# Kernel tuning notes

Hardware: AMD Instinct MI355X
Metric: run time of the kernel (lower is better)

The kernel has to match this reference:

```python
import jax, jax.numpy as jnp
import numpy as np
from jax import lax

POST_NMS_TOP_N = 1000   # cfg[cfg_key].RPN_POST_NMS_TOP_N
NMS_THRESH = 0.7        # cfg[cfg_key].RPN_NMS_THRESH
NEG = -1e9
B, N = 4, 65536


def setup_inputs() -> dict:
    key = jax.random.key(0)
    k0, k1, k2, k3, k4, k5, k6 = jax.random.split(key, 7)
    scores = jax.random.uniform(k0, (B, N), dtype=jnp.float32)
    # small deltas so exp(dw) stays in a realistic range
    bbox_deltas = 0.1 * jax.random.normal(k1, (B, N, 4), dtype=jnp.float32)
    # plausible anchor boxes inside a 1024x1024 image
    cx = jax.random.uniform(k2, (N,), minval=0.0, maxval=1024.0)
    cy = jax.random.uniform(k3, (N,), minval=0.0, maxval=1024.0)
    w = jax.random.uniform(k4, (N,), minval=16.0, maxval=256.0)
    h = jax.random.uniform(k5, (N,), minval=16.0, maxval=256.0)
    anchors = jnp.stack([cx - 0.5 * w, cy - 0.5 * h, cx + 0.5 * w, cy + 0.5 * h], axis=-1).astype(jnp.float32)
    im_info = jnp.tile(jnp.array([[1024.0, 1024.0, 1.0]], dtype=jnp.float32), (B, 1))
    ids = jax.random.randint(k6, (N,), 0, 5, dtype=jnp.int32)  # FPN level ids
    return {"scores": scores, "bbox_deltas": bbox_deltas, "anchors": anchors,
            "im_info": im_info, "ids": ids}


def _iou_one(box, boxes):
    # box [4], boxes [N,4]; mmcv convention (no +1)
    x1 = jnp.maximum(box[0], boxes[:, 0])
    y1 = jnp.maximum(box[1], boxes[:, 1])
    x2 = jnp.minimum(box[2], boxes[:, 2])
    y2 = jnp.minimum(box[3], boxes[:, 3])
    inter = jnp.clip(x2 - x1, 0.0) * jnp.clip(y2 - y1, 0.0)
    a1 = (box[2] - box[0]) * (box[3] - box[1])
    a2 = (boxes[:, 2] - boxes[:, 0]) * (boxes[:, 3] - boxes[:, 1])
    return inter / jnp.maximum(a1 + a2 - inter, 1e-6)


def _nms_single(boxes, scores, ids):
    # batched_nms: offset boxes by level id so levels never suppress each other
    max_c = jnp.max(boxes) + 1.0
    boxes_off = boxes + (ids.astype(boxes.dtype) * max_c)[:, None]

    def step(s, _):
        i = jnp.argmax(s)
        valid = s[i] > NEG * 0.5
        iou = _iou_one(boxes_off[i], boxes_off)
        s_new = jnp.where(iou > NMS_THRESH, NEG, s).at[i].set(NEG)
        sel = jnp.where(valid, boxes[i], jnp.zeros((4,), boxes.dtype))
        return s_new, sel

    _, sel = lax.scan(step, scores, None, length=POST_NMS_TOP_N)
    return sel  # [POST_NMS_TOP_N, 4], in descending score order (as batched_nms returns)


def _forward(scores, bbox_deltas, anchors, im_info, ids):
    ws = anchors[:, 2] - anchors[:, 0] + 1.0          # [N]
    hs = anchors[:, 3] - anchors[:, 1] + 1.0
    ctr_x = anchors[:, 0] + 0.5 * ws
    ctr_y = anchors[:, 1] + 0.5 * hs
    dx, dy, dw, dh = (bbox_deltas[..., 0], bbox_deltas[..., 1],
                      bbox_deltas[..., 2], bbox_deltas[..., 3])  # [B,N]
    pcx = dx * ws + ctr_x
    pcy = dy * hs + ctr_y
    pw = jnp.exp(dw) * ws
    ph = jnp.exp(dh) * hs
    proposals = jnp.stack([pcx - 0.5 * pw, pcy - 0.5 * ph,
                           pcx + 0.5 * pw, pcy + 0.5 * ph], axis=-1)  # [B,N,4]
    # clip_boxes: x in [0, w-1], y in [0, h-1]
    wmax = im_info[:, 1][:, None] - 1.0
    hmax = im_info[:, 0][:, None] - 1.0
    x1 = jnp.clip(proposals[..., 0], 0.0, wmax)
    y1 = jnp.clip(proposals[..., 1], 0.0, hmax)
    x2 = jnp.clip(proposals[..., 2], 0.0, wmax)
    y2 = jnp.clip(proposals[..., 3], 0.0, hmax)
    proposals = jnp.stack([x1, y1, x2, y2], axis=-1)
    # per-image batched NMS (greedy descending-score selection == sort + NMS)
    sel = jax.vmap(_nms_single, in_axes=(0, 0, None))(proposals, scores, ids)  # [B,topN,4]
    batch_col = jnp.broadcast_to(
        jnp.arange(scores.shape[0], dtype=sel.dtype)[:, None, None],
        (scores.shape[0], POST_NMS_TOP_N, 1))
    return jnp.concatenate([batch_col, sel], axis=-1)  # [B,topN,5]


def reference(scores, bbox_deltas, anchors, im_info, ids):
    return _forward(scores, bbox_deltas, anchors, im_info, ids)
```

## Files before the change

### kernel.cpp

```cpp
#include <hip/hip_runtime.h>
#include <stdint.h>

#define NB     65536
#define BATCH  4
#define TOPN   1000
#define MMAX   2048
#define NTILE  (MMAX / 64)
#define NPAIRS (NTILE * (NTILE + 1) / 2)
#define CAP    128
#define KSUP   8
#define UNC    128
#define THRESH 0.974f
#define NEGV   (-1e9f)
#define NMS_T  0.7f

#define OFF_CBLK   64
#define OFF_KRAW   1088
#define OFF_SBOX   263232
#define OFF_SLEV   394304
#define OFF_CNT2   427072
#define OFF_SUP    459840

__device__ __forceinline__ void decode_box(const float4* __restrict__ anchors4,
                                           const float4* __restrict__ deltas4,
                                           int b, int i, float wmax, float hmax,
                                           float& x1, float& y1, float& x2, float& y2) {
  float4 a = anchors4[i];
  float4 d = deltas4[(size_t)b * NB + i];
  float ws = a.z - a.x + 1.0f;
  float hs = a.w - a.y + 1.0f;
  float cx = a.x + 0.5f * ws;
  float cy = a.y + 0.5f * hs;
  float pcx = d.x * ws + cx;
  float pcy = d.y * hs + cy;
  float pw = expf(d.z) * ws;
  float ph = expf(d.w) * hs;
  x1 = pcx - 0.5f * pw; y1 = pcy - 0.5f * ph;
  x2 = pcx + 0.5f * pw; y2 = pcy + 0.5f * ph;
  x1 = fminf(fmaxf(x1, 0.0f), wmax);
  y1 = fminf(fmaxf(y1, 0.0f), hmax);
  x2 = fminf(fmaxf(x2, 0.0f), wmax);
  y2 = fminf(fmaxf(y2, 0.0f), hmax);
}

__device__ __forceinline__ uint32_t blockscan(uint32_t v, volatile uint32_t* wsum,
                                              int tid, uint32_t* total) {
  __syncthreads();
  int lane = tid & 63, wid = tid >> 6;
  uint32_t x = v;
  for (int off = 1; off < 64; off <<= 1) {
    uint32_t u = __shfl_up(x, off, 64);
    if (lane >= off) x += u;
  }
  if (lane == 63) wsum[wid] = x;
  __syncthreads();
  if (tid == 0) {
    uint32_t run = 0;
    for (int w = 0; w < 4; ++w) { uint32_t t = wsum[w]; wsum[w] = run; run += t; }
    wsum[4] = run;
  }
  __syncthreads();
  *total = wsum[4];
  return x - v + wsum[wid];
}

__global__ __launch_bounds__(256) void k_prep(const float* __restrict__ scores,
                                              unsigned long long* __restrict__ keys_raw,
                                              uint32_t* __restrict__ cnt_blk) {
  const int b = blockIdx.x >> 6;
  const int blk = blockIdx.x & 63;
  const int tid = threadIdx.x;
  __shared__ uint32_t wsum[5];
  const float4* s4 = (const float4*)scores + (size_t)b * (NB / 4) + (size_t)blk * 256 + tid;
  float4 s = *s4;
  float sc4[4] = {s.x, s.y, s.z, s.w};
  uint32_t cmask = 0, ccount = 0;
#pragma unroll
  for (int k = 0; k < 4; ++k)
    if (sc4[k] >= THRESH) { cmask |= (1u << k); ccount++; }
  uint32_t total;
  uint32_t p = blockscan(ccount, wsum, tid, &total);
  if (tid == 0) cnt_blk[blockIdx.x] = total;
  unsigned long long* dst = keys_raw + (size_t)blockIdx.x * CAP;
#pragma unroll
  for (int k = 0; k < 4; ++k) {
    if (cmask & (1u << k)) {
      if (p < (uint32_t)CAP) {
        int i = (blk << 10) + (tid << 2) + k;
        dst[p] = ((unsigned long long)(~__float_as_uint(sc4[k])) << 32) | (uint32_t)i;
      }
      p++;
    }
  }
}

__global__ __launch_bounds__(256) void k_rank(const uint32_t* __restrict__ cnt_blk,
                                              const unsigned long long* __restrict__ keys_raw,
                                              const float4* __restrict__ deltas4,
                                              const float4* __restrict__ anchors4,
                                              const float* __restrict__ im_info,
                                              const int* __restrict__ ids,
                                              uint32_t* ctrs,
                                              float4* sboxes, int* slev,
                                              uint32_t* cnt2) {
  const int b = blockIdx.y;
  const int r = blockIdx.x;
  const int tid = threadIdx.x;
  const int lane = tid & 63, wid = tid >> 6;
  __shared__ unsigned long long sk[MMAX];
  __shared__ uint32_t scnt[64], sbs[64];
  __shared__ uint32_t psum[256];
  __shared__ uint32_t meta[2];

  if (tid < 64) {
    uint32_t c = cnt_blk[b * 64 + tid];
    uint32_t cc = min(c, (uint32_t)CAP);
    scnt[tid] = cc;
    uint32_t x = cc;
    for (int off = 1; off < 64; off <<= 1) {
      uint32_t u = __shfl_up(x, off, 64);
      if (lane >= off) x += u;
    }
    sbs[tid] = x - cc;
    unsigned long long ov = __ballot(c > (uint32_t)CAP);
    if (tid == 63) { meta[0] = x; meta[1] = (ov != 0ULL) ? 1u : 0u; }
  }
  __syncthreads();
  uint32_t nsum = meta[0];
  int n = min((int)nsum, MMAX);
  uint32_t flag = meta[1] | ((nsum > (uint32_t)MMAX) ? 1u : 0u);
  if (r == 0 && tid == 0) {
    ctrs[b] = (uint32_t)n;
    ctrs[8 + b] = flag;
  }
  if (tid < 64) cnt2[(size_t)b * MMAX + r * 64 + tid] = 0u;
  {
    int k = tid >> 2, q = tid & 3;
    uint32_t cb = sbs[k], cc = scnt[k];
    const unsigned long long* src = keys_raw + ((size_t)b * 64 + k) * CAP;
    for (uint32_t o = q; o < cc; o += 4) {
      uint32_t d = cb + o;
      if (d < (uint32_t)MMAX) sk[d] = src[o];
    }
  }
  for (int i = tid; i < MMAX; i += 256) if (i >= n) sk[i] = ~0ULL;
  __syncthreads();
  int c = r * 64 + lane;
  uint32_t partial = 0;
  if (c < n) {
    unsigned long long myk = sk[c];
    const ulonglong2* p2 = (const ulonglong2*)(sk + (size_t)wid * 512);
    for (int it = 0; it < 256; it += 4) {
      ulonglong2 a = p2[it], bq = p2[it + 1], cq = p2[it + 2], dq = p2[it + 3];
      partial += (uint32_t)(a.x < myk) + (uint32_t)(a.y < myk) +
                 (uint32_t)(bq.x < myk) + (uint32_t)(bq.y < myk) +
                 (uint32_t)(cq.x < myk) + (uint32_t)(cq.y < myk) +
                 (uint32_t)(dq.x < myk) + (uint32_t)(dq.y < myk);
    }
  }
  psum[wid * 64 + lane] = partial;
  __syncthreads();
  if (tid < 64) {
    int cc = r * 64 + tid;
    if (cc < n) {
      uint32_t rank = psum[tid] + psum[64 + tid] + psum[128 + tid] + psum[192 + tid];
      if (rank < (uint32_t)MMAX) {
        unsigned long long key = sk[cc];
        int i = (int)(uint32_t)key;
        float wmax = im_info[b * 3 + 1] - 1.0f;
        float hmax = im_info[b * 3 + 0] - 1.0f;
        float x1, y1, x2, y2;
        decode_box(anchors4, deltas4, b, i, wmax, hmax, x1, y1, x2, y2);
        sboxes[(size_t)b * MMAX + rank] = make_float4(x1, y1, x2, y2);
        slev[(size_t)b * MMAX + rank] = ids[i];
      }
    }
  }
}

__global__ __launch_bounds__(64) void k_pairs(uint32_t* ctrs,
                                              const float4* __restrict__ sboxes,
                                              const int* __restrict__ slev,
                                              uint32_t* cnt2, int* suplist) {
  int b = blockIdx.y;
  int p = blockIdx.x;
  int tj = (int)((sqrtf(8.0f * (float)p + 1.0f) - 1.0f) * 0.5f);
  while ((tj + 1) * (tj + 2) / 2 <= p) ++tj;
  while (tj * (tj + 1) / 2 > p) --tj;
  int ti = p - tj * (tj + 1) / 2;
  int n = min((int)ctrs[b], MMAX);
  if (tj * 64 >= n) return;
  int lane = threadIdx.x;

  __shared__ float4 ib[64];
  __shared__ int il[64];
  int ii = ti * 64 + lane;
  if (ii < n) {
    ib[lane] = sboxes[(size_t)b * MMAX + ii];
    il[lane] = slev[(size_t)b * MMAX + ii];
  } else {
    il[lane] = -1;
  }
  int j = tj * 64 + lane;
  float4 J = make_float4(0.f, 0.f, 0.f, 0.f);
  int jl = -2;
  float aj = 0.0f;
  if (j < n) {
    J = sboxes[(size_t)b * MMAX + j];
    jl = slev[(size_t)b * MMAX + j];
    aj = (J.z - J.x) * (J.w - J.y);
  }
  __syncthreads();
  if (j < n) {
    int imax = (ti == tj) ? lane : 64;
    for (int k = 0; k < imax; ++k) {
      if (il[k] != jl) continue;
      float4 I = ib[k];
      float xx1 = fmaxf(I.x, J.x), yy1 = fmaxf(I.y, J.y);
      float xx2 = fminf(I.z, J.z), yy2 = fminf(I.w, J.w);
      float inter = fmaxf(xx2 - xx1, 0.0f) * fmaxf(yy2 - yy1, 0.0f);
      float ai = (I.z - I.x) * (I.w - I.y);
      float iou = inter / fmaxf((ai + aj) - inter, 1e-6f);
      if (iou > NMS_T) {
        uint32_t s = atomicAdd(&cnt2[(size_t)b * MMAX + j], 1u);
        if (s < (uint32_t)KSUP) suplist[((size_t)b * MMAX + j) * KSUP + s] = ti * 64 + k;
        else ctrs[8 + b] = 1u;
      }
    }
  }
}

__device__ __forceinline__ uint32_t scan_pair(uint32_t pairsum, volatile uint32_t* wsum,
                                              int tid, uint32_t* total_out) {
  int lane = tid & 63, wid = tid >> 6;
  uint32_t v = pairsum;
  for (int off = 1; off < 64; off <<= 1) {
    uint32_t u = __shfl_up(v, off, 64);
    if (lane >= off) v += u;
  }
  if (lane == 63) wsum[wid] = v;
  __syncthreads();
  if (tid == 0) {
    uint32_t run = 0;
    for (int w = 0; w < 16; ++w) { uint32_t t = wsum[w]; wsum[w] = run; run += t; }
    wsum[16] = run;
  }
  __syncthreads();
  uint32_t incl = v + wsum[wid];
  *total_out = wsum[16];
  return incl - pairsum;
}

__global__ __launch_bounds__(1024) void k_out(const float* __restrict__ scores,
                                              const float4* __restrict__ deltas4,
                                              const float4* __restrict__ anchors4,
                                              const float* __restrict__ im_info,
                                              const int* __restrict__ ids,
                                              const uint32_t* __restrict__ ctrs,
                                              const uint32_t* __restrict__ cnt2,
                                              const int* __restrict__ suplist,
                                              const float4* __restrict__ sboxes,
                                              float* __restrict__ out) {
  int b = blockIdx.x;
  int tid = threadIdx.x;
  __shared__ uint8_t kept[MMAX];
  __shared__ uint32_t wsum[17];
  __shared__ uint16_t unc[UNC];
  __shared__ int supld[UNC][KSUP];
  __shared__ uint8_t supn[UNC];
  int n = min((int)ctrs[b], MMAX);
  int j0 = tid * 2, j1 = tid * 2 + 1;
  uint32_t c0 = (j0 < n) ? cnt2[(size_t)b * MMAX + j0] : 0u;
  uint32_t c1 = (j1 < n) ? cnt2[(size_t)b * MMAX + j1] : 0u;
  kept[j0] = (j0 < n && c0 == 0u) ? 1 : 0;
  kept[j1] = (j1 < n && c1 == 0u) ? 1 : 0;
  uint32_t u0 = (j0 < n && c0 > 0u) ? 1u : 0u;
  uint32_t u1 = (j1 < n && c1 > 0u) ? 1u : 0u;
  uint32_t tot_unc;
  uint32_t base = scan_pair(u0 + u1, wsum, tid, &tot_unc);
  if (u0) {
    uint32_t p = base;
    if (p < UNC) {
      int m = (int)min(c0, (uint32_t)KSUP);
      unc[p] = (uint16_t)j0; supn[p] = (uint8_t)m;
      for (int s = 0; s < m; ++s) supld[p][s] = suplist[((size_t)b * MMAX + j0) * KSUP + s];
    }
  }
  if (u1) {
    uint32_t p = base + u0;
    if (p < UNC) {
      int m = (int)min(c1, (uint32_t)KSUP);
      unc[p] = (uint16_t)j1; supn[p] = (uint8_t)m;
      for (int s = 0; s < m; ++s) supld[p][s] = suplist[((size_t)b * MMAX + j1) * KSUP + s];
    }
  }
  __syncthreads();
  if (tid < 64) {
    int nu = (int)min(tot_unc, (uint32_t)UNC);
    for (int u = 0; u < nu; ++u) {
      int m = (int)supn[u];
      int pred = (tid < m) ? (int)kept[supld[u][tid]] : 0;
      unsigned long long bal = __ballot(pred);
      if (tid == 0) kept[unc[u]] = (bal == 0ULL) ? 1 : 0;
    }
  }
  __syncthreads();
  uint32_t k0 = kept[j0], k1 = kept[j1];
  uint32_t total;
  uint32_t pbase = scan_pair(k0 + k1, wsum, tid, &total);
  if (k0 && pbase < (uint32_t)TOPN) {
    float4 bx = sboxes[(size_t)b * MMAX + j0];
    size_t o = ((size_t)b * TOPN + pbase) * 5;
    out[o] = (float)b; out[o+1] = bx.x; out[o+2] = bx.y; out[o+3] = bx.z; out[o+4] = bx.w;
  }
  if (k1) {
    uint32_t p = pbase + k0;
    if (p < (uint32_t)TOPN) {
      float4 bx = sboxes[(size_t)b * MMAX + j1];
      size_t o = ((size_t)b * TOPN + p) * 5;
      out[o] = (float)b; out[o+1] = bx.x; out[o+2] = bx.y; out[o+3] = bx.z; out[o+4] = bx.w;
    }
  }
  for (int t = tid; t < TOPN; t += 1024) {
    if ((uint32_t)t >= total) {
      size_t o = ((size_t)b * TOPN + t) * 5;
      out[o] = (float)b; out[o+1] = 0.0f; out[o+2] = 0.0f; out[o+3] = 0.0f; out[o+4] = 0.0f;
    }
  }

  bool needFB = (ctrs[8 + b] != 0u) || (total < (uint32_t)TOPN) || (tot_unc > (uint32_t)UNC);
  if (!needFB) return;

  __shared__ uint32_t mask[NB / 32];
  __shared__ float rv[1024];
  __shared__ int ri[1024];
  __shared__ float fm[16];
  const float wmax = im_info[b * 3 + 1] - 1.0f;
  const float hmax = im_info[b * 3 + 0] - 1.0f;
  __syncthreads();
  float mx = 0.0f;
  for (int i = tid; i < NB; i += 1024) {
    float x1, y1, x2, y2;
    decode_box(anchors4, deltas4, b, i, wmax, hmax, x1, y1, x2, y2);
    mx = fmaxf(mx, fmaxf(fmaxf(x1, y1), fmaxf(x2, y2)));
  }
  for (int o = 32; o > 0; o >>= 1) mx = fmaxf(mx, __shfl_xor(mx, o, 64));
  if ((tid & 63) == 0) fm[tid >> 6] = mx;
  __syncthreads();
  if (tid == 0) {
    float m = fm[0];
    for (int w = 1; w < 16; ++w) m = fmaxf(m, fm[w]);
    fm[0] = m;
  }
  for (int i = tid; i < NB / 32; i += 1024) mask[i] = 0u;
  __syncthreads();
  float max_c = fm[0] + 1.0f;
  for (int it = 0; it < TOPN; ++it) {
    float bv = -3e38f; int bi = 0x7fffffff;
    for (int i = tid; i < NB; i += 1024) {
      bool sup = (mask[i >> 5] >> (i & 31)) & 1u;
      float v = sup ? NEGV : scores[(size_t)b * NB + i];
      if (v > bv || (v == bv && i < bi)) { bv = v; bi = i; }
    }
    rv[tid] = bv; ri[tid] = bi;
    __syncthreads();
    for (int s = 512; s > 0; s >>= 1) {
      if (tid < s) {
        float v2 = rv[tid + s]; int i2 = ri[tid + s];
        if (v2 > rv[tid] || (v2 == rv[tid] && i2 < ri[tid])) { rv[tid] = v2; ri[tid] = i2; }
      }
      __syncthreads();
    }
    int ii = ri[0]; float vv = rv[0];
    bool valid = vv > NEGV * 0.5f;
    if (!valid) {
      if (tid == 0) {
        size_t o = ((size_t)b * TOPN + it) * 5;
        out[o] = (float)b; out[o+1] = 0; out[o+2] = 0; out[o+3] = 0; out[o+4] = 0;
      }
      __syncthreads();
      continue;
    }
    float x1, y1, x2, y2;
    decode_box(anchors4, deltas4, b, ii, wmax, hmax, x1, y1, x2, y2);
    int lv = ids[ii];
    float off = (float)lv * max_c;
    float s0 = x1 + off, s1 = y1 + off, s2 = x2 + off, s3 = y2 + off;
    float a1 = (s2 - s0) * (s3 - s1);
    if (tid == 0) {
      size_t o = ((size_t)b * TOPN + it) * 5;
      out[o] = (float)b; out[o+1] = x1; out[o+2] = y1; out[o+3] = x2; out[o+4] = y2;
    }
    for (int j = tid; j < NB; j += 1024) {
      if ((mask[j >> 5] >> (j & 31)) & 1u) continue;
      if (ids[j] != lv) continue;
      float bx1, by1, bx2, by2;
      decode_box(anchors4, deltas4, b, j, wmax, hmax, bx1, by1, bx2, by2);
      float t0 = bx1 + off, t1 = by1 + off, t2 = bx2 + off, t3 = by2 + off;
      float xx1 = fmaxf(s0, t0), yy1 = fmaxf(s1, t1);
      float xx2 = fminf(s2, t2), yy2 = fminf(s3, t3);
      float inter = fmaxf(xx2 - xx1, 0.0f) * fmaxf(yy2 - yy1, 0.0f);
      float a2r = (t2 - t0) * (t3 - t1);
      float iou = inter / fmaxf(a1 + a2r - inter, 1e-6f);
      if (iou > NMS_T) atomicOr(&mask[j >> 5], 1u << (j & 31));
    }
    if (tid == 0) atomicOr(&mask[ii >> 5], 1u << (ii & 31));
    __syncthreads();
  }
}

extern "C" void kernel_launch(void* const* d_in, const int* in_sizes, int n_in,
                              void* d_out, int out_size, void* d_ws, size_t ws_size,
                              hipStream_t stream) {
  const float*  scores   = (const float*)d_in[0];
  const float4* deltas4  = (const float4*)d_in[1];
  const float4* anchors4 = (const float4*)d_in[2];
  const float*  im_info  = (const float*)d_in[3];
  const int*    ids      = (const int*)d_in[4];
  float* out = (float*)d_out;

  char* ws = (char*)d_ws;
  uint32_t*           ctrs     = (uint32_t*)ws;
  uint32_t*           cnt_blk  = (uint32_t*)(ws + OFF_CBLK);
  unsigned long long* keys_raw = (unsigned long long*)(ws + OFF_KRAW);
  float4*             sboxes   = (float4*)(ws + OFF_SBOX);
  int*                slev     = (int*)(ws + OFF_SLEV);
  uint32_t*           cnt2     = (uint32_t*)(ws + OFF_CNT2);
  int*                suplist  = (int*)(ws + OFF_SUP);

  hipLaunchKernelGGL(k_prep, dim3(64 * BATCH), dim3(256), 0, stream,
                     scores, keys_raw, cnt_blk);
  hipLaunchKernelGGL(k_rank, dim3(NTILE, BATCH), dim3(256), 0, stream,
                     cnt_blk, keys_raw, deltas4, anchors4, im_info, ids,
                     ctrs, sboxes, slev, cnt2);
  hipLaunchKernelGGL(k_pairs, dim3(NPAIRS, BATCH), dim3(64), 0, stream,
                     ctrs, sboxes, slev, cnt2, suplist);
  hipLaunchKernelGGL(k_out, dim3(BATCH), dim3(1024), 0, stream,
                     scores, deltas4, anchors4, im_info, ids, ctrs, cnt2, suplist,
                     sboxes, out);
}
```

Measured before the change: 101.0 us.

## Fuse pairwise IoU kernel with output kernel via last-block-done counter

Merges the pairwise suppression kernel and the per-image output/resolution kernel into one launch. Each 1024-thread block handles 16 tile pairs, one per wave, then increments a per-image counter; the last block to finish runs the kept-resolution and output stage. This removes one kernel launch and its inter-kernel gap, at the cost of threadfences, atomic loads, and larger blocks that hold extra shared memory and may run at lower occupancy.

```diff
diff --git a/kernel.cpp b/kernel.cpp
--- a/kernel.cpp
+++ b/kernel.cpp
@@ -7,6 +7,7 @@
 #define MMAX   2048
 #define NTILE  (MMAX / 64)
 #define NPAIRS (NTILE * (NTILE + 1) / 2)
+#define PBLK   (NPAIRS / 16)
 #define CAP    128
 #define KSUP   8
 #define UNC    128
@@ -132,6 +133,7 @@
   if (r == 0 && tid == 0) {
     ctrs[b] = (uint32_t)n;
     ctrs[8 + b] = flag;
+    ctrs[12 + b] = 0u;
   }
   if (tid < 64) cnt2[(size_t)b * MMAX + r * 64 + tid] = 0u;
   {
@@ -178,58 +180,6 @@
   }
 }
 
-__global__ __launch_bounds__(64) void k_pairs(uint32_t* ctrs,
-                                              const float4* __restrict__ sboxes,
-                                              const int* __restrict__ slev,
-                                              uint32_t* cnt2, int* suplist) {
-  int b = blockIdx.y;
-  int p = blockIdx.x;
-  int tj = (int)((sqrtf(8.0f * (float)p + 1.0f) - 1.0f) * 0.5f);
-  while ((tj + 1) * (tj + 2) / 2 <= p) ++tj;
-  while (tj * (tj + 1) / 2 > p) --tj;
-  int ti = p - tj * (tj + 1) / 2;
-  int n = min((int)ctrs[b], MMAX);
-  if (tj * 64 >= n) return;
-  int lane = threadIdx.x;
-
-  __shared__ float4 ib[64];
-  __shared__ int il[64];
-  int ii = ti * 64 + lane;
-  if (ii < n) {
-    ib[lane] = sboxes[(size_t)b * MMAX + ii];
-    il[lane] = slev[(size_t)b * MMAX + ii];
-  } else {
-    il[lane] = -1;
-  }
-  int j = tj * 64 + lane;
-  float4 J = make_float4(0.f, 0.f, 0.f, 0.f);
-  int jl = -2;
-  float aj = 0.0f;
-  if (j < n) {
-    J = sboxes[(size_t)b * MMAX + j];
-    jl = slev[(size_t)b * MMAX + j];
-    aj = (J.z - J.x) * (J.w - J.y);
-  }
-  __syncthreads();
-  if (j < n) {
-    int imax = (ti == tj) ? lane : 64;
-    for (int k = 0; k < imax; ++k) {
-      if (il[k] != jl) continue;
-      float4 I = ib[k];
-      float xx1 = fmaxf(I.x, J.x), yy1 = fmaxf(I.y, J.y);
-      float xx2 = fminf(I.z, J.z), yy2 = fminf(I.w, J.w);
-      float inter = fmaxf(xx2 - xx1, 0.0f) * fmaxf(yy2 - yy1, 0.0f);
-      float ai = (I.z - I.x) * (I.w - I.y);
-      float iou = inter / fmaxf((ai + aj) - inter, 1e-6f);
-      if (iou > NMS_T) {
-        uint32_t s = atomicAdd(&cnt2[(size_t)b * MMAX + j], 1u);
-        if (s < (uint32_t)KSUP) suplist[((size_t)b * MMAX + j) * KSUP + s] = ti * 64 + k;
-        else ctrs[8 + b] = 1u;
-      }
-    }
-  }
-}
-
 __device__ __forceinline__ uint32_t scan_pair(uint32_t pairsum, volatile uint32_t* wsum,
                                               int tid, uint32_t* total_out) {
   int lane = tid & 63, wid = tid >> 6;
@@ -251,27 +201,85 @@
   return incl - pairsum;
 }
 
-__global__ __launch_bounds__(1024) void k_out(const float* __restrict__ scores,
-                                              const float4* __restrict__ deltas4,
-                                              const float4* __restrict__ anchors4,
-                                              const float* __restrict__ im_info,
-                                              const int* __restrict__ ids,
-                                              const uint32_t* __restrict__ ctrs,
-                                              const uint32_t* __restrict__ cnt2,
-                                              const int* __restrict__ suplist,
-                                              const float4* __restrict__ sboxes,
-                                              float* __restrict__ out) {
-  int b = blockIdx.x;
-  int tid = threadIdx.x;
+__global__ __launch_bounds__(1024) void k_po(const float* __restrict__ scores,
+                                             const float4* __restrict__ deltas4,
+                                             const float4* __restrict__ anchors4,
+                                             const float* __restrict__ im_info,
+                                             const int* __restrict__ ids,
+                                             uint32_t* ctrs,
+                                             const float4* __restrict__ sboxes,
+                                             const int* __restrict__ slev,
+                                             uint32_t* cnt2, int* suplist,
+                                             float* __restrict__ out) {
+  const int b = blockIdx.y;
+  const int blkL = blockIdx.x;
+  const int tid = threadIdx.x;
+  const int lane = tid & 63, wid = tid >> 6;
+  __shared__ float4 ib[16][64];
+  __shared__ int il[16][64];
+  __shared__ int swin;
+  int n = min((int)ctrs[b], MMAX);
+
+  {
+    int p = blkL * 16 + wid;
+    int tj = (int)((sqrtf(8.0f * (float)p + 1.0f) - 1.0f) * 0.5f);
+    while ((tj + 1) * (tj + 2) / 2 <= p) ++tj;
+    while (tj * (tj + 1) / 2 > p) --tj;
+    int ti = p - tj * (tj + 1) / 2;
+    bool act = (tj * 64 < n);
+    int ii = ti * 64 + lane;
+    if (act && ii < n) {
+      ib[wid][lane] = sboxes[(size_t)b * MMAX + ii];
+      il[wid][lane] = slev[(size_t)b * MMAX + ii];
+    } else {
+      il[wid][lane] = -1;
+    }
+    int j = tj * 64 + lane;
+    float4 J = make_float4(0.f, 0.f, 0.f, 0.f);
+    int jl = -2;
+    float aj = 0.0f;
+    if (act && j < n) {
+      J = sboxes[(size_t)b * MMAX + j];
+      jl = slev[(size_t)b * MMAX + j];
+      aj = (J.z - J.x) * (J.w - J.y);
+    }
+    __syncthreads();
+    if (act && j < n) {
+      int imax = (ti == tj) ? lane : 64;
+      for (int k = 0; k < imax; ++k) {
+        if (il[wid][k] != jl) continue;
+        float4 I = ib[wid][k];
+        float xx1 = fmaxf(I.x, J.x), yy1 = fmaxf(I.y, J.y);
+        float xx2 = fminf(I.z, J.z), yy2 = fminf(I.w, J.w);
+        float inter = fmaxf(xx2 - xx1, 0.0f) * fmaxf(yy2 - yy1, 0.0f);
+        float ai = (I.z - I.x) * (I.w - I.y);
+        float iou = inter / fmaxf((ai + aj) - inter, 1e-6f);
+        if (iou > NMS_T) {
+          uint32_t s = atomicAdd(&cnt2[(size_t)b * MMAX + j], 1u);
+          if (s < (uint32_t)KSUP) suplist[((size_t)b * MMAX + j) * KSUP + s] = ti * 64 + k;
+          else atomicOr(&ctrs[8 + b], 1u);
+        }
+      }
+    }
+  }
+
+  __threadfence();
+  __syncthreads();
+  if (tid == 0) swin = ((int)atomicAdd(&ctrs[12 + b], 1u) == PBLK - 1) ? 1 : 0;
+  __syncthreads();
+  if (!swin) return;
+  __threadfence();
+
   __shared__ uint8_t kept[MMAX];
   __shared__ uint32_t wsum[17];
   __shared__ uint16_t unc[UNC];
   __shared__ int supld[UNC][KSUP];
   __shared__ uint8_t supn[UNC];
-  int n = min((int)ctrs[b], MMAX);
   int j0 = tid * 2, j1 = tid * 2 + 1;
-  uint32_t c0 = (j0 < n) ? cnt2[(size_t)b * MMAX + j0] : 0u;
-  uint32_t c1 = (j1 < n) ? cnt2[(size_t)b * MMAX + j1] : 0u;
+  uint32_t c0 = (j0 < n) ? __hip_atomic_load(&cnt2[(size_t)b * MMAX + j0],
+                                             __ATOMIC_RELAXED, __HIP_MEMORY_SCOPE_AGENT) : 0u;
+  uint32_t c1 = (j1 < n) ? __hip_atomic_load(&cnt2[(size_t)b * MMAX + j1],
+                                             __ATOMIC_RELAXED, __HIP_MEMORY_SCOPE_AGENT) : 0u;
   kept[j0] = (j0 < n && c0 == 0u) ? 1 : 0;
   kept[j1] = (j1 < n && c1 == 0u) ? 1 : 0;
   uint32_t u0 = (j0 < n && c0 > 0u) ? 1u : 0u;
@@ -283,7 +291,9 @@
     if (p < UNC) {
       int m = (int)min(c0, (uint32_t)KSUP);
       unc[p] = (uint16_t)j0; supn[p] = (uint8_t)m;
-      for (int s = 0; s < m; ++s) supld[p][s] = suplist[((size_t)b * MMAX + j0) * KSUP + s];
+      for (int s = 0; s < m; ++s)
+        supld[p][s] = __hip_atomic_load(&suplist[((size_t)b * MMAX + j0) * KSUP + s],
+                                        __ATOMIC_RELAXED, __HIP_MEMORY_SCOPE_AGENT);
     }
   }
   if (u1) {
@@ -291,7 +301,9 @@
     if (p < UNC) {
       int m = (int)min(c1, (uint32_t)KSUP);
       unc[p] = (uint16_t)j1; supn[p] = (uint8_t)m;
-      for (int s = 0; s < m; ++s) supld[p][s] = suplist[((size_t)b * MMAX + j1) * KSUP + s];
+      for (int s = 0; s < m; ++s)
+        supld[p][s] = __hip_atomic_load(&suplist[((size_t)b * MMAX + j1) * KSUP + s],
+                                        __ATOMIC_RELAXED, __HIP_MEMORY_SCOPE_AGENT);
     }
   }
   __syncthreads();
@@ -328,7 +340,8 @@
     }
   }
 
-  bool needFB = (ctrs[8 + b] != 0u) || (total < (uint32_t)TOPN) || (tot_unc > (uint32_t)UNC);
+  uint32_t gflag = __hip_atomic_load(&ctrs[8 + b], __ATOMIC_RELAXED, __HIP_MEMORY_SCOPE_AGENT);
+  bool needFB = (gflag != 0u) || (total < (uint32_t)TOPN) || (tot_unc > (uint32_t)UNC);
   if (!needFB) return;
 
   __shared__ uint32_t mask[NB / 32];
@@ -433,9 +446,7 @@
   hipLaunchKernelGGL(k_rank, dim3(NTILE, BATCH), dim3(256), 0, stream,
                      cnt_blk, keys_raw, deltas4, anchors4, im_info, ids,
                      ctrs, sboxes, slev, cnt2);
-  hipLaunchKernelGGL(k_pairs, dim3(NPAIRS, BATCH), dim3(64), 0, stream,
-                     ctrs, sboxes, slev, cnt2, suplist);
-  hipLaunchKernelGGL(k_out, dim3(BATCH), dim3(1024), 0, stream,
-                     scores, deltas4, anchors4, im_info, ids, ctrs, cnt2, suplist,
-                     sboxes, out);
-}
+  hipLaunchKernelGGL(k_po, dim3(PBLK, BATCH), dim3(1024), 0, stream,
+                     scores, deltas4, anchors4, im_info, ids, ctrs,
+                     sboxes, slev, cnt2, suplist, out);
+}
```

Result: slower. 128.6 us (+27.2%).
